# Optimization experiments

Measured on AMD Instinct MI355X. Metric: run time of the kernel, lower is better.

The kernel has to match this reference:

```python
import jax, jax.numpy as jnp
import numpy as np

N = 50000      # nodes
E = 1600000    # edges
R = 12         # relations (num_unique_edge_attrs)
F_IN = 64      # num_node_features
H = 128        # hidden_channels
C = 10         # num_classes
G = 256        # graphs in batch
EPS = 1e-5     # BatchNorm eps


def setup_inputs() -> dict:
    key = jax.random.key(0)
    ks = jax.random.split(key, 10)
    s = 0.05
    return {
        "x": jax.random.normal(ks[0], (N, F_IN), jnp.float32),
        "Wrel1": jax.random.normal(ks[1], (R, F_IN, H), jnp.float32) * s,
        "root1": jax.random.normal(ks[2], (F_IN, H), jnp.float32) * s,
        "bias1": jnp.zeros((H,), jnp.float32),
        "gamma1": jnp.ones((H,), jnp.float32),
        "beta1": jnp.zeros((H,), jnp.float32),
        "Wrel2": jax.random.normal(ks[3], (R, H, H), jnp.float32) * s,
        "root2": jax.random.normal(ks[4], (H, H), jnp.float32) * s,
        "bias2": jnp.zeros((H,), jnp.float32),
        "gamma2": jnp.ones((H,), jnp.float32),
        "beta2": jnp.zeros((H,), jnp.float32),
        "Wf": jax.random.normal(ks[5], (H, C), jnp.float32) * s,
        "bf": jnp.zeros((C,), jnp.float32),
        "edge_index": jax.random.randint(ks[6], (2, E), 0, N, dtype=jnp.int64) if jax.config.jax_enable_x64 else jax.random.randint(ks[6], (2, E), 0, N),
        "edge_type": jax.random.randint(ks[7], (E,), 0, R),
        "batch": jnp.sort(jax.random.randint(ks[8], (N,), 0, G)),
    }


def _segment_mean(vals, idx, num):
    # mean aggregation; empty segments -> 0
    s = jax.ops.segment_sum(vals, idx, num_segments=num)
    c = jax.ops.segment_sum(jnp.ones(idx.shape, vals.dtype), idx, num_segments=num)
    return s / jnp.clip(c, 1.0)[:, None]


def _rgcn(x, Wrel, root, bias, src, dst, edge_type):
    # PyG RGCNConv with aggr='mean': per-relation mean of source features, then W_r
    seg = dst * R + edge_type                      # fused (node, relation) segment id
    h = _segment_mean(x[src], seg, N * R)          # [N*R, in]
    h = h.reshape(N, R, x.shape[1])
    return jnp.einsum('nri,rio->no', h, Wrel) + x @ root + bias


def _bn(x, gamma, beta):
    # BatchNorm1d training-mode math (batch statistics, biased variance)
    mu = jnp.mean(x, axis=0)
    var = jnp.mean((x - mu) ** 2, axis=0)
    return gamma * (x - mu) / jnp.sqrt(var + EPS) + beta


def reference(x, Wrel1, root1, bias1, gamma1, beta1,
              Wrel2, root2, bias2, gamma2, beta2,
              Wf, bf, edge_index, edge_type, batch):
    src, dst = edge_index[0], edge_index[1]
    h = jax.nn.relu(_bn(_rgcn(x, Wrel1, root1, bias1, src, dst, edge_type), gamma1, beta1))
    h = jax.nn.relu(_bn(_rgcn(h, Wrel2, root2, bias2, src, dst, edge_type), gamma2, beta2))
    pooled = _segment_mean(h, batch, G)            # global_mean_pool -> [G, H]
    return pooled @ Wf + bf                        # [G, C]
```

## Files before the change

### kernel.cpp

```cpp
#include <hip/hip_runtime.h>

constexpr int N_NODES = 50000;
constexpr int N_EDGES = 1600000;
constexpr int NREL    = 12;
constexpr int F_INPUT = 64;
constexpr int HID     = 128;
constexpr int NCLS    = 10;
constexpr int NGRAPH  = 256;
constexpr int NSEG    = N_NODES * NREL;
constexpr float BN_EPS = 1e-5f;

constexpr int NB    = 391;
constexpr int SEGB  = 128 * NREL;
constexpr int NBLK  = 392;
constexpr int PTPB  = 1024;
constexpr int EPB   = 4096;

typedef float v4f __attribute__((ext_vector_type(4)));
typedef short s8b __attribute__((ext_vector_type(8)));

__device__ __forceinline__ unsigned f2bf(float f) {
    unsigned u = __float_as_uint(f);
    return (u + 0x7FFFu + ((u >> 16) & 1u)) >> 16;
}
__device__ __forceinline__ unsigned pack2(float a, float b) {
    return f2bf(a) | (f2bf(b) << 16);
}

constexpr int PQ0 = 64;
constexpr int PQ1 = PQ0 + 64;
constexpr int PQ2 = PQ1 + 8192;
constexpr int PQ3 = PQ2 + 13 * F_INPUT * HID;
constexpr int PQ4 = PQ3 + 13 * HID * HID;
constexpr int PQ5 = PQ4 + N_NODES * F_INPUT / 4;
constexpr int PQ6 = PQ5 + NGRAPH;
constexpr int PREP_BLOCKS = (PQ6 + 255) / 256;

__global__ void prep(const float* __restrict__ Wrel1, const float* __restrict__ root1,
                     const float* __restrict__ Wrel2, const float* __restrict__ root2,
                     const float* __restrict__ x, const int* __restrict__ batch,
                     ushort* __restrict__ Wp1, ushort* __restrict__ Wp2,
                     ushort* __restrict__ xb,
                     float* __restrict__ bn1, float* __restrict__ bn2,
                     float* __restrict__ psum, float* __restrict__ pcnt) {
    int tid = blockIdx.x * 256 + threadIdx.x;
    const uint4 z = make_uint4(0, 0, 0, 0);
    if (tid < PQ0) { reinterpret_cast<uint4*>(bn1)[tid] = z; return; }
    if (tid < PQ1) { reinterpret_cast<uint4*>(bn2)[tid - PQ0] = z; return; }
    if (tid < PQ2) { reinterpret_cast<uint4*>(psum)[tid - PQ1] = z; return; }
    if (tid < PQ3) {
        int idx = tid - PQ2;
        int r = idx >> 13, rem = idx & 8191;
        int k = rem >> 7, n = rem & 127;
        const float* W = (r < NREL) ? (Wrel1 + (size_t)r * 8192) : root1;
        float v = W[k * HID + n];
        int b = k >> 5, kk = k & 31;
        int j = (n & 7) * 16 + (n >> 3);
        Wp1[(((size_t)(r * 2 + b)) * HID + j) * 32 + kk] = (ushort)f2bf(v);
        return;
    }
    if (tid < PQ4) {
        int idx = tid - PQ3;
        int r = idx >> 14, rem = idx & 16383;
        int k = rem >> 7, n = rem & 127;
        const float* W = (r < NREL) ? (Wrel2 + (size_t)r * 16384) : root2;
        float v = W[k * HID + n];
        int b = k >> 5, kk = k & 31;
        int j = (n & 7) * 16 + (n >> 3);
        Wp2[(((size_t)(r * 4 + b)) * HID + j) * 32 + kk] = (ushort)f2bf(v);
        return;
    }
    if (tid < PQ5) {
        int i = tid - PQ4;
        float4 v = reinterpret_cast<const float4*>(x)[i];
        uint2 o;
        o.x = pack2(v.x, v.y);
        o.y = pack2(v.z, v.w);
        reinterpret_cast<uint2*>(xb)[i] = o;
        return;
    }
    if (tid < PQ6) {
        int g = tid - PQ5;
        int lo0 = 0, hi0 = N_NODES;
        while (lo0 < hi0) { int m = (lo0 + hi0) >> 1; if (batch[m] < g) lo0 = m + 1; else hi0 = m; }
        int lo1 = lo0, hi1 = N_NODES;
        while (lo1 < hi1) { int m = (lo1 + hi1) >> 1; if (batch[m] < g + 1) lo1 = m + 1; else hi1 = m; }
        pcnt[g] = (float)(lo1 - lo0);
    }
}


__global__ __launch_bounds__(PTPB)
void part_hist(const int* __restrict__ dst, int* __restrict__ histG) {
    __shared__ int h[NB];
    int t = threadIdx.x, blk = blockIdx.x;
    if (t < NB) h[t] = 0;
    __syncthreads();
    int base = blk * EPB;
#pragma unroll
    for (int it = 0; it < EPB / PTPB; ++it) {
        int e = base + it * PTPB + t;
        if (e < N_EDGES) atomicAdd(&h[dst[e] >> 7], 1);
    }
    __syncthreads();
    if (t < NB) histG[blk * NB + t] = h[t];
}

__global__ __launch_bounds__(512)
void part_scanA(const int* __restrict__ histG, int* __restrict__ cursorG,
                int* __restrict__ bucketTot) {
    __shared__ int s[512];
    int t = threadIdx.x, b = blockIdx.x;
    int v = (t < NBLK) ? histG[t * NB + b] : 0;
    s[t] = v;
    __syncthreads();
    for (int d = 1; d < 512; d <<= 1) {
        int x = (t >= d) ? s[t - d] : 0;
        __syncthreads();
        s[t] += x;
        __syncthreads();
    }
    if (t < NBLK) cursorG[t * NB + b] = s[t] - v;
    if (t == NBLK - 1) bucketTot[b] = s[t];
}

__global__ __launch_bounds__(512)
void part_scanB(const int* __restrict__ bucketTot, int* __restrict__ bucketBase) {
    __shared__ int s[512];
    int t = threadIdx.x;
    int v = (t < NB) ? bucketTot[t] : 0;
    s[t] = v;
    __syncthreads();
    for (int d = 1; d < 512; d <<= 1) {
        int x = (t >= d) ? s[t - d] : 0;
        __syncthreads();
        s[t] += x;
        __syncthreads();
    }
    if (t <= NB) bucketBase[t] = (t == 0) ? 0 : s[t - 1];
}

__global__ __launch_bounds__(PTPB)
void part_scatter(const int* __restrict__ src, const int* __restrict__ dst,
                  const int* __restrict__ et, const int* __restrict__ cursorG,
                  const int* __restrict__ bucketBase, uint* __restrict__ ebuck) {
    __shared__ int cur[NB];
    int t = threadIdx.x, blk = blockIdx.x;
    if (t < NB) cur[t] = cursorG[blk * NB + t] + bucketBase[t];
    __syncthreads();
    int base = blk * EPB;
#pragma unroll
    for (int it = 0; it < EPB / PTPB; ++it) {
        int e = base + it * PTPB + t;
        if (e < N_EDGES) {
            int d = dst[e];
            int b = d >> 7;
            int pos = atomicAdd(&cur[b], 1);
            ebuck[pos] = (uint)src[e] | ((uint)(d & 127) << 16) | ((uint)et[e] << 23);
        }
    }
}

__global__ __launch_bounds__(256)
void csr_finalize(const uint* __restrict__ ebuck, const int* __restrict__ bucketBase,
                  int* __restrict__ off, int* __restrict__ zrow, float* __restrict__ wgt) {
    __shared__ int cnt[SEGB];
    __shared__ int cur[SEGB];
    __shared__ float winv[SEGB];
    __shared__ int partial[256];
    int t = threadIdx.x, b = blockIdx.x;
    int eb0 = bucketBase[b], eb1 = bucketBase[b + 1];
#pragma unroll
    for (int i = 0; i < 6; ++i) cnt[t * 6 + i] = 0;
    __syncthreads();
    for (int e = eb0 + t; e < eb1; e += 256) {
        uint u = ebuck[e];
        int key = (int)((u >> 16) & 127) * NREL + (int)(u >> 23);
        atomicAdd(&cnt[key], 1);
    }
    __syncthreads();
    int loc[6];
    int sum = 0;
#pragma unroll
    for (int i = 0; i < 6; ++i) { loc[i] = sum; sum += cnt[t * 6 + i]; }
    partial[t] = sum;
    __syncthreads();
    for (int d = 1; d < 256; d <<= 1) {
        int v = (t >= d) ? partial[t - d] : 0;
        __syncthreads();
        partial[t] += v;
        __syncthreads();
    }
    int tbase = (t == 0) ? 0 : partial[t - 1];
    int nodeb = b * 128;
#pragma unroll
    for (int i = 0; i < 6; ++i) {
        int s = t * 6 + i;
        int gpos = eb0 + tbase + loc[i];
        cur[s] = gpos;
        int c = cnt[s];
        winv[s] = (c > 0) ? 1.0f / (float)c : 0.f;
        int node = nodeb + s / NREL;
        if (node < N_NODES) off[node * NREL + (s % NREL)] = gpos;
    }
    __syncthreads();
    for (int e = eb0 + t; e < eb1; e += 256) {
        uint u = ebuck[e];
        int key = (int)((u >> 16) & 127) * NREL + (int)(u >> 23);
        int pos = atomicAdd(&cur[key], 1);
        zrow[pos] = (int)(u >> 23) * N_NODES + (int)(u & 0xFFFFu);
        wgt[pos] = winv[key];
    }
    if (b == 0 && t == 0) off[NSEG] = N_EDGES;
}


template <int F>
__launch_bounds__(256)
__global__ void gemm_rel(const ushort* __restrict__ xin, const ushort* __restrict__ Wp,
                         ushort* __restrict__ Z) {
    constexpr int FP2 = F + 8;
    constexpr int KB  = F / 32;
    constexpr int CHW = F / 4;
    constexpr int NLD = CHW / 8;
    __shared__ __align__(16) ushort A[64 * FP2];
    const int t = threadIdx.x;
    const int n0 = blockIdx.x * 64;
    const int nl = t >> 2, tid4 = t & 3;
    const int lane = t & 63, wave = t >> 6, q = lane >> 4, l16 = lane & 15;

    {
        int n = n0 + nl;
        uint4* dst = reinterpret_cast<uint4*>(A + nl * FP2 + tid4 * CHW);
        if (n < N_NODES) {
            const uint4* srcp =
                reinterpret_cast<const uint4*>(xin + (size_t)n * F + tid4 * CHW);
#pragma unroll
            for (int c = 0; c < NLD; ++c) dst[c] = srcp[c];
        } else {
            uint4 z = make_uint4(0, 0, 0, 0);
#pragma unroll
            for (int c = 0; c < NLD; ++c) dst[c] = z;
        }
    }
    __syncthreads();

    s8b afr[KB];
    const ushort* Arow = A + (wave * 16 + l16) * FP2 + q * 8;
#pragma unroll
    for (int b = 0; b < KB; ++b)
        afr[b] = *reinterpret_cast<const s8b*>(Arow + b * 32);

    const int rowb = n0 + wave * 16 + q * 4;
    for (int rel = 0; rel < 13; ++rel) {
        v4f acc[8];
#pragma unroll
        for (int nt = 0; nt < 8; ++nt) acc[nt] = (v4f){0.f, 0.f, 0.f, 0.f};
#pragma unroll
        for (int b = 0; b < KB; ++b) {
            const ushort* wb = Wp + ((size_t)(rel * KB + b) * HID + l16) * 32 + q * 8;
#pragma unroll
            for (int nt = 0; nt < 8; ++nt) {
                s8b bfb = *reinterpret_cast<const s8b*>(wb + (size_t)nt * 16 * 32);
                acc[nt] = __builtin_amdgcn_mfma_f32_16x16x32_bf16(afr[b], bfb, acc[nt], 0, 0, 0);
            }
        }
        ushort* zr = Z + (size_t)rel * ((size_t)N_NODES * HID);
#pragma unroll
        for (int rr = 0; rr < 4; ++rr) {
            int n = rowb + rr;
            if (n < N_NODES) {
                uint4 o;
                o.x = pack2(acc[0][rr], acc[1][rr]);
                o.y = pack2(acc[2][rr], acc[3][rr]);
                o.z = pack2(acc[4][rr], acc[5][rr]);
                o.w = pack2(acc[6][rr], acc[7][rr]);
                *reinterpret_cast<uint4*>(zr + (size_t)n * HID + l16 * 8) = o;
            }
        }
    }
}


__launch_bounds__(256)
__global__ void agg_bn(const ushort* __restrict__ Z, const int* __restrict__ off,
                       const int* __restrict__ zrow, const float* __restrict__ wgt,
                       const float* __restrict__ bias,
                       float* __restrict__ H, float* __restrict__ bn_sum,
                       float* __restrict__ bn_sq) {
    __shared__ float RED[2][4][HID];
    const int t = threadIdx.x;
    const int lane = t & 63, wave = t >> 6;
    const int n0 = blockIdx.x * 32 + wave * 8;
    const float2 bv = *reinterpret_cast<const float2*>(bias + lane * 2);
    float ps0 = 0.f, ps1 = 0.f, pq0 = 0.f, pq1 = 0.f;

    for (int i = 0; i < 8; ++i) {
        int n = n0 + i;
        if (n >= N_NODES) break;
        int e0 = off[n * NREL];
        int ee = off[n * NREL + NREL];
        uint ur = *reinterpret_cast<const uint*>(
            Z + ((size_t)12 * N_NODES + n) * HID + lane * 2);
        float a0 = __uint_as_float(ur << 16) + bv.x;
        float a1 = __uint_as_float(ur & 0xFFFF0000u) + bv.y;
        int elast = ee - 1;
        for (int e = e0; e < ee; e += 8) {
            int zr_[8];
            float w_[8];
#pragma unroll
            for (int j = 0; j < 8; ++j) {
                int ec = min(e + j, elast);
                zr_[j] = zrow[ec];
                w_[j] = (e + j < ee) ? wgt[ec] : 0.f;
            }
            uint u_[8];
#pragma unroll
            for (int j = 0; j < 8; ++j)
                u_[j] = *reinterpret_cast<const uint*>(
                    Z + (size_t)zr_[j] * HID + lane * 2);
#pragma unroll
            for (int j = 0; j < 8; ++j) {
                a0 += __uint_as_float(u_[j] << 16) * w_[j];
                a1 += __uint_as_float(u_[j] & 0xFFFF0000u) * w_[j];
            }
        }
        *reinterpret_cast<float2*>(H + (size_t)n * HID + lane * 2) = make_float2(a0, a1);
        ps0 += a0; ps1 += a1;
        pq0 += a0 * a0; pq1 += a1 * a1;
    }
    RED[0][wave][lane * 2] = ps0; RED[0][wave][lane * 2 + 1] = ps1;
    RED[1][wave][lane * 2] = pq0; RED[1][wave][lane * 2 + 1] = pq1;
    __syncthreads();
    {
        int stat = t >> 7, col = t & 127;
        float v = RED[stat][0][col] + RED[stat][1][col] +
                  RED[stat][2][col] + RED[stat][3][col];
        if (stat == 0) atomicAdd(&bn_sum[col], v);
        else           atomicAdd(&bn_sq[col], v);
    }
}


__global__ void bn_relu_bf16(const float* __restrict__ h, const float* __restrict__ bn_sum,
                             const float* __restrict__ bn_sq, const float* __restrict__ gamma,
                             const float* __restrict__ beta, ushort* __restrict__ outb) {
    __shared__ float CA[HID], CB[HID];
    int t = threadIdx.x;
    if (t < HID) {
        float mu = bn_sum[t] * (1.0f / N_NODES);
        float var = bn_sq[t] * (1.0f / N_NODES) - mu * mu;
        float a = gamma[t] / sqrtf(var + BN_EPS);
        CA[t] = a;
        CB[t] = beta[t] - a * mu;
    }
    __syncthreads();
    int i = blockIdx.x * 256 + t;
    constexpr int TOTAL = N_NODES * HID / 4;
    if (i < TOTAL) {
        int o4 = i & 31;
        float4 a = reinterpret_cast<const float4*>(CA)[o4];
        float4 b = reinterpret_cast<const float4*>(CB)[o4];
        float4 v = reinterpret_cast<const float4*>(h)[i];
        v.x = fmaxf(a.x * v.x + b.x, 0.f);
        v.y = fmaxf(a.y * v.y + b.y, 0.f);
        v.z = fmaxf(a.z * v.z + b.z, 0.f);
        v.w = fmaxf(a.w * v.w + b.w, 0.f);
        uint2 o;
        o.x = pack2(v.x, v.y);
        o.y = pack2(v.z, v.w);
        reinterpret_cast<uint2*>(outb)[i] = o;
    }
}


__global__ void pool_bnrelu(const float* __restrict__ h, const float* __restrict__ bn_sum,
                            const float* __restrict__ bn_sq, const float* __restrict__ gamma,
                            const float* __restrict__ beta, const int* __restrict__ batch,
                            float* __restrict__ psum) {
    __shared__ float CA[HID], CB[HID];
    int t = threadIdx.x;
    if (t < HID) {
        float mu = bn_sum[t] * (1.0f / N_NODES);
        float var = bn_sq[t] * (1.0f / N_NODES) - mu * mu;
        float a = gamma[t] / sqrtf(var + BN_EPS);
        CA[t] = a;
        CB[t] = beta[t] - a * mu;
    }
    __syncthreads();
    int col = t & 127;
    int nb = blockIdx.x * 16 + (t >> 7) * 8;
    float a = CA[col], b = CB[col];
    float run = 0.f;
    int curg = -1;
    for (int i = 0; i < 8; ++i) {
        int n = nb + i;
        if (n < N_NODES) {
            int g = batch[n];
            float v = fmaxf(a * h[(size_t)n * HID + col] + b, 0.f);
            if (g != curg) {
                if (curg >= 0) atomicAdd(&psum[curg * HID + col], run);
                run = 0.f;
                curg = g;
            }
            run += v;
        }
    }
    if (curg >= 0) atomicAdd(&psum[curg * HID + col], run);
}

__global__ void final_kernel(const float* __restrict__ psum, const float* __restrict__ pcnt,
                             const float* __restrict__ Wf, const float* __restrict__ bf,
                             float* __restrict__ out) {
    __shared__ float p[HID];
    int g = blockIdx.x, t = threadIdx.x;
    float inv = 1.0f / fmaxf(pcnt[g], 1.0f);
    p[t] = psum[g * HID + t] * inv;
    p[t + 64] = psum[g * HID + t + 64] * inv;
    __syncthreads();
    if (t < NCLS) {
        float s = bf[t];
#pragma unroll 16
        for (int k = 0; k < HID; ++k) s += p[k] * Wf[k * NCLS + t];
        out[g * NCLS + t] = s;
    }
}


extern "C" void kernel_launch(void* const* d_in, const int* in_sizes, int n_in,
                              void* d_out, int out_size, void* d_ws, size_t ws_size,
                              hipStream_t stream) {
    const float* x      = (const float*)d_in[0];
    const float* Wrel1  = (const float*)d_in[1];
    const float* root1  = (const float*)d_in[2];
    const float* bias1  = (const float*)d_in[3];
    const float* gamma1 = (const float*)d_in[4];
    const float* beta1  = (const float*)d_in[5];
    const float* Wrel2  = (const float*)d_in[6];
    const float* root2  = (const float*)d_in[7];
    const float* bias2  = (const float*)d_in[8];
    const float* gamma2 = (const float*)d_in[9];
    const float* beta2  = (const float*)d_in[10];
    const float* Wf     = (const float*)d_in[11];
    const float* bf     = (const float*)d_in[12];
    const int* ei       = (const int*)d_in[13];
    const int* et       = (const int*)d_in[14];
    const int* batch    = (const int*)d_in[15];
    const int* srcv = ei;
    const int* dstv = ei + N_EDGES;

    char* w = (char*)d_ws;
    auto alloc = [&](size_t bytes) -> char* {
        char* p = w;
        w += (bytes + 255) / 256 * 256;
        return p;
    };
    int* off     = (int*)alloc((size_t)(NSEG + 1) * 4);
    int* zrow    = (int*)alloc((size_t)N_EDGES * 4);
    float* wgt   = (float*)alloc((size_t)N_EDGES * 4);
    ushort* xb   = (ushort*)alloc((size_t)N_NODES * F_INPUT * 2);
    ushort* H1b  = (ushort*)alloc((size_t)N_NODES * HID * 2);
    ushort* Wp1  = (ushort*)alloc((size_t)13 * F_INPUT * HID * 2);
    ushort* Wp2  = (ushort*)alloc((size_t)13 * HID * HID * 2);
    float* bn1   = (float*)alloc(2 * HID * 4);
    float* bn2   = (float*)alloc(2 * HID * 4);
    float* psum  = (float*)alloc((size_t)NGRAPH * HID * 4);
    float* pcnt  = (float*)alloc((size_t)NGRAPH * 4);
    float* Hbuf  = (float*)alloc((size_t)N_NODES * HID * 4);
    char* ovl    = alloc((size_t)13 * N_NODES * HID * 2);
    int* histG      = (int*)ovl;
    int* cursorG    = (int*)(ovl + (size_t)NBLK * NB * 4);
    int* bucketTot  = (int*)(ovl + (size_t)2 * NBLK * NB * 4);
    int* bucketBase = (int*)(ovl + (size_t)2 * NBLK * NB * 4 + (NB + 1) * 4 + 252);
    uint* ebuck     = (uint*)(ovl + (size_t)2 * NBLK * NB * 4 + 4096);
    ushort* Zb      = (ushort*)ovl;

    prep<<<PREP_BLOCKS, 256, 0, stream>>>(Wrel1, root1, Wrel2, root2, x, batch,
                                          Wp1, Wp2, xb, bn1, bn2, psum, pcnt);

    part_hist<<<NBLK, PTPB, 0, stream>>>(dstv, histG);
    part_scanA<<<NB, 512, 0, stream>>>(histG, cursorG, bucketTot);
    part_scanB<<<1, 512, 0, stream>>>(bucketTot, bucketBase);
    part_scatter<<<NBLK, PTPB, 0, stream>>>(srcv, dstv, et, cursorG, bucketBase, ebuck);
    csr_finalize<<<NB, 256, 0, stream>>>(ebuck, bucketBase, off, zrow, wgt);

    int gblk = (N_NODES + 63) / 64;
    int ablk = (N_NODES + 31) / 32;

    gemm_rel<F_INPUT><<<gblk, 256, 0, stream>>>(xb, Wp1, Zb);
    agg_bn<<<ablk, 256, 0, stream>>>(Zb, off, zrow, wgt, bias1, Hbuf, bn1, bn1 + HID);
    bn_relu_bf16<<<(N_NODES * HID / 4 + 255) / 256, 256, 0, stream>>>(Hbuf, bn1, bn1 + HID,
                                                                      gamma1, beta1, H1b);

    gemm_rel<HID><<<gblk, 256, 0, stream>>>(H1b, Wp2, Zb);
    agg_bn<<<ablk, 256, 0, stream>>>(Zb, off, zrow, wgt, bias2, Hbuf, bn2, bn2 + HID);

    pool_bnrelu<<<(N_NODES + 15) / 16, 256, 0, stream>>>(Hbuf, bn2, bn2 + HID, gamma2, beta2,
                                                         batch, psum);
    final_kernel<<<NGRAPH, 64, 0, stream>>>(psum, pcnt, Wf, bf, (float*)d_out);
}
```

Baseline: 556.4 us.

## Split relation transforms into two passes to shrink the gathered Z buffer

Each RGCN layer's per-relation transform and gather-aggregation now runs in two halves: relations 0-5, then relations 6-11 plus the root term. This shrinks the bf16 Z buffer from 13 to 7 relation slabs, so the random gathers hit a smaller working set that fits better in cache. The cost is two extra kernel launches per layer, re-reading the input features for the second GEMM, and an extra read-modify-write of the fp32 H buffer.

```diff
diff --git a/kernel.cpp b/kernel.cpp
--- a/kernel.cpp
+++ b/kernel.cpp
@@ -9,6 +9,9 @@
 constexpr int NGRAPH  = 256;
 constexpr int NSEG    = N_NODES * NREL;
 constexpr float BN_EPS = 1e-5f;
+
+constexpr int NRELA = 6;
+constexpr int NRELB = 7;
 
 constexpr int NB    = 391;
 constexpr int SEGB  = 128 * NREL;
@@ -206,16 +209,18 @@
     __syncthreads();
     for (int e = eb0 + t; e < eb1; e += 256) {
         uint u = ebuck[e];
-        int key = (int)((u >> 16) & 127) * NREL + (int)(u >> 23);
+        int rel = (int)(u >> 23);
+        int key = (int)((u >> 16) & 127) * NREL + rel;
         int pos = atomicAdd(&cur[key], 1);
-        zrow[pos] = (int)(u >> 23) * N_NODES + (int)(u & 0xFFFFu);
+        int relc = (rel < NRELA) ? rel : rel - NRELA;
+        zrow[pos] = relc * N_NODES + (int)(u & 0xFFFFu);
         wgt[pos] = winv[key];
     }
     if (b == 0 && t == 0) off[NSEG] = N_EDGES;
 }
 
 
-template <int F>
+template <int F, int NR>
 __launch_bounds__(256)
 __global__ void gemm_rel(const ushort* __restrict__ xin, const ushort* __restrict__ Wp,
                          ushort* __restrict__ Z) {
@@ -252,7 +257,7 @@
         afr[b] = *reinterpret_cast<const s8b*>(Arow + b * 32);
 
     const int rowb = n0 + wave * 16 + q * 4;
-    for (int rel = 0; rel < 13; ++rel) {
+    for (int rel = 0; rel < NR; ++rel) {
         v4f acc[8];
 #pragma unroll
         for (int nt = 0; nt < 8; ++nt) acc[nt] = (v4f){0.f, 0.f, 0.f, 0.f};
@@ -282,6 +287,7 @@
 }
 
 
+template <bool FIRST>
 __launch_bounds__(256)
 __global__ void agg_bn(const ushort* __restrict__ Z, const int* __restrict__ off,
                        const int* __restrict__ zrow, const float* __restrict__ wgt,
@@ -292,47 +298,61 @@
     const int t = threadIdx.x;
     const int lane = t & 63, wave = t >> 6;
     const int n0 = blockIdx.x * 32 + wave * 8;
-    const float2 bv = *reinterpret_cast<const float2*>(bias + lane * 2);
+    const float2 bv = FIRST ? make_float2(0.f, 0.f)
+                            : *reinterpret_cast<const float2*>(bias + lane * 2);
     float ps0 = 0.f, ps1 = 0.f, pq0 = 0.f, pq1 = 0.f;
 
     for (int i = 0; i < 8; ++i) {
         int n = n0 + i;
         if (n >= N_NODES) break;
-        int e0 = off[n * NREL];
-        int ee = off[n * NREL + NREL];
-        uint ur = *reinterpret_cast<const uint*>(
-            Z + ((size_t)12 * N_NODES + n) * HID + lane * 2);
-        float a0 = __uint_as_float(ur << 16) + bv.x;
-        float a1 = __uint_as_float(ur & 0xFFFF0000u) + bv.y;
-        int elast = ee - 1;
-        for (int e = e0; e < ee; e += 8) {
-            int zr_[8];
-            float w_[8];
-#pragma unroll
-            for (int j = 0; j < 8; ++j) {
-                int ec = min(e + j, elast);
-                zr_[j] = zrow[ec];
-                w_[j] = (e + j < ee) ? wgt[ec] : 0.f;
+        int e0, ee;
+        float a0, a1;
+        if (FIRST) {
+            e0 = off[n * NREL];
+            ee = off[n * NREL + NRELA];
+            a0 = 0.f; a1 = 0.f;
+        } else {
+            e0 = off[n * NREL + NRELA];
+            ee = off[n * NREL + NREL];
+            float2 hp = *reinterpret_cast<const float2*>(H + (size_t)n * HID + lane * 2);
+            uint ur = *reinterpret_cast<const uint*>(
+                Z + ((size_t)6 * N_NODES + n) * HID + lane * 2);
+            a0 = hp.x + __uint_as_float(ur << 16) + bv.x;
+            a1 = hp.y + __uint_as_float(ur & 0xFFFF0000u) + bv.y;
+        }
+        if (e0 < ee) {
+            int elast = ee - 1;
+            for (int e = e0; e < ee; e += 8) {
+                int zr_[8];
+                float w_[8];
+#pragma unroll
+                for (int j = 0; j < 8; ++j) {
+                    int ec = min(e + j, elast);
+                    zr_[j] = zrow[ec];
+                    w_[j] = (e + j < ee) ? wgt[ec] : 0.f;
+                }
+                uint u_[8];
+#pragma unroll
+                for (int j = 0; j < 8; ++j)
+                    u_[j] = *reinterpret_cast<const uint*>(
+                        Z + (size_t)zr_[j] * HID + lane * 2);
+#pragma unroll
+                for (int j = 0; j < 8; ++j) {
+                    a0 += __uint_as_float(u_[j] << 16) * w_[j];
+                    a1 += __uint_as_float(u_[j] & 0xFFFF0000u) * w_[j];
+                }
             }
-            uint u_[8];
-#pragma unroll
-            for (int j = 0; j < 8; ++j)
-                u_[j] = *reinterpret_cast<const uint*>(
-                    Z + (size_t)zr_[j] * HID + lane * 2);
-#pragma unroll
-            for (int j = 0; j < 8; ++j) {
-                a0 += __uint_as_float(u_[j] << 16) * w_[j];
-                a1 += __uint_as_float(u_[j] & 0xFFFF0000u) * w_[j];
-            }
         }
         *reinterpret_cast<float2*>(H + (size_t)n * HID + lane * 2) = make_float2(a0, a1);
-        ps0 += a0; ps1 += a1;
-        pq0 += a0 * a0; pq1 += a1 * a1;
-    }
-    RED[0][wave][lane * 2] = ps0; RED[0][wave][lane * 2 + 1] = ps1;
-    RED[1][wave][lane * 2] = pq0; RED[1][wave][lane * 2 + 1] = pq1;
-    __syncthreads();
-    {
+        if (!FIRST) {
+            ps0 += a0; ps1 += a1;
+            pq0 += a0 * a0; pq1 += a1 * a1;
+        }
+    }
+    if (!FIRST) {
+        RED[0][wave][lane * 2] = ps0; RED[0][wave][lane * 2 + 1] = ps1;
+        RED[1][wave][lane * 2] = pq0; RED[1][wave][lane * 2 + 1] = pq1;
+        __syncthreads();
         int stat = t >> 7, col = t & 127;
         float v = RED[stat][0][col] + RED[stat][1][col] +
                   RED[stat][2][col] + RED[stat][3][col];
@@ -467,7 +487,7 @@
     float* psum  = (float*)alloc((size_t)NGRAPH * HID * 4);
     float* pcnt  = (float*)alloc((size_t)NGRAPH * 4);
     float* Hbuf  = (float*)alloc((size_t)N_NODES * HID * 4);
-    char* ovl    = alloc((size_t)13 * N_NODES * HID * 2);
+    char* ovl    = alloc((size_t)NRELB * N_NODES * HID * 2);
     int* histG      = (int*)ovl;
     int* cursorG    = (int*)(ovl + (size_t)NBLK * NB * 4);
     int* bucketTot  = (int*)(ovl + (size_t)2 * NBLK * NB * 4);
@@ -487,13 +507,20 @@
     int gblk = (N_NODES + 63) / 64;
     int ablk = (N_NODES + 31) / 32;
 
-    gemm_rel<F_INPUT><<<gblk, 256, 0, stream>>>(xb, Wp1, Zb);
-    agg_bn<<<ablk, 256, 0, stream>>>(Zb, off, zrow, wgt, bias1, Hbuf, bn1, bn1 + HID);
+    const size_t WOFF1 = (size_t)NRELA * (F_INPUT / 32) * HID * 32;
+    const size_t WOFF2 = (size_t)NRELA * (HID / 32) * HID * 32;
+
+    gemm_rel<F_INPUT, NRELA><<<gblk, 256, 0, stream>>>(xb, Wp1, Zb);
+    agg_bn<true><<<ablk, 256, 0, stream>>>(Zb, off, zrow, wgt, bias1, Hbuf, bn1, bn1 + HID);
+    gemm_rel<F_INPUT, NRELB><<<gblk, 256, 0, stream>>>(xb, Wp1 + WOFF1, Zb);
+    agg_bn<false><<<ablk, 256, 0, stream>>>(Zb, off, zrow, wgt, bias1, Hbuf, bn1, bn1 + HID);
     bn_relu_bf16<<<(N_NODES * HID / 4 + 255) / 256, 256, 0, stream>>>(Hbuf, bn1, bn1 + HID,
                                                                       gamma1, beta1, H1b);
 
-    gemm_rel<HID><<<gblk, 256, 0, stream>>>(H1b, Wp2, Zb);
-    agg_bn<<<ablk, 256, 0, stream>>>(Zb, off, zrow, wgt, bias2, Hbuf, bn2, bn2 + HID);
+    gemm_rel<HID, NRELA><<<gblk, 256, 0, stream>>>(H1b, Wp2, Zb);
+    agg_bn<true><<<ablk, 256, 0, stream>>>(Zb, off, zrow, wgt, bias2, Hbuf, bn2, bn2 + HID);
+    gemm_rel<HID, NRELB><<<gblk, 256, 0, stream>>>(H1b, Wp2 + WOFF2, Zb);
+    agg_bn<false><<<ablk, 256, 0, stream>>>(Zb, off, zrow, wgt, bias2, Hbuf, bn2, bn2 + HID);
 
     pool_bnrelu<<<(N_NODES + 15) / 16, 256, 0, stream>>>(Hbuf, bn2, bn2 + HID, gamma2, beta2,
                                                          batch, psum);
```

Result: slower. 591.6 us (+6.3%).

## Reorder RGCN to aggregate inputs first, then single concatenated GEMM with fused BN stats

Applied to the files above, without the earlier changes.

Instead of computing per-relation transformed features for all nodes and gathering them per edge, the code now computes per-(node,relation) means of the raw input features into a concatenated matrix and multiplies it by stacked weights in one GEMM. Bias and BatchNorm statistics are fused into the GEMM epilogue, and the CSR no longer stores per-edge weights or relation-offset row indices. Gathers now hit a small input array instead of the large 13-slice Z buffer, improving cache locality, at the cost of writing and reading a large concatenated intermediate and a longer-K GEMM.

```diff
diff --git a/kernel.cpp b/kernel.cpp
--- a/kernel.cpp
+++ b/kernel.cpp
@@ -163,10 +163,9 @@
 
 __global__ __launch_bounds__(256)
 void csr_finalize(const uint* __restrict__ ebuck, const int* __restrict__ bucketBase,
-                  int* __restrict__ off, int* __restrict__ zrow, float* __restrict__ wgt) {
+                  int* __restrict__ off, int* __restrict__ esrc) {
     __shared__ int cnt[SEGB];
     __shared__ int cur[SEGB];
-    __shared__ float winv[SEGB];
     __shared__ int partial[256];
     int t = threadIdx.x, b = blockIdx.x;
     int eb0 = bucketBase[b], eb1 = bucketBase[b + 1];
@@ -198,8 +197,6 @@
         int s = t * 6 + i;
         int gpos = eb0 + tbase + loc[i];
         cur[s] = gpos;
-        int c = cnt[s];
-        winv[s] = (c > 0) ? 1.0f / (float)c : 0.f;
         int node = nodeb + s / NREL;
         if (node < N_NODES) off[node * NREL + (s % NREL)] = gpos;
     }
@@ -208,8 +205,7 @@
         uint u = ebuck[e];
         int key = (int)((u >> 16) & 127) * NREL + (int)(u >> 23);
         int pos = atomicAdd(&cur[key], 1);
-        zrow[pos] = (int)(u >> 23) * N_NODES + (int)(u & 0xFFFFu);
-        wgt[pos] = winv[key];
+        esrc[pos] = (int)(u & 0xFFFFu);
     }
     if (b == 0 && t == 0) off[NSEG] = N_EDGES;
 }
@@ -217,125 +213,140 @@
 
 template <int F>
 __launch_bounds__(256)
-__global__ void gemm_rel(const ushort* __restrict__ xin, const ushort* __restrict__ Wp,
-                         ushort* __restrict__ Z) {
-    constexpr int FP2 = F + 8;
-    constexpr int KB  = F / 32;
-    constexpr int CHW = F / 4;
-    constexpr int NLD = CHW / 8;
-    __shared__ __align__(16) ushort A[64 * FP2];
-    const int t = threadIdx.x;
-    const int n0 = blockIdx.x * 64;
-    const int nl = t >> 2, tid4 = t & 3;
-    const int lane = t & 63, wave = t >> 6, q = lane >> 4, l16 = lane & 15;
-
-    {
-        int n = n0 + nl;
-        uint4* dst = reinterpret_cast<uint4*>(A + nl * FP2 + tid4 * CHW);
-        if (n < N_NODES) {
-            const uint4* srcp =
-                reinterpret_cast<const uint4*>(xin + (size_t)n * F + tid4 * CHW);
-#pragma unroll
-            for (int c = 0; c < NLD; ++c) dst[c] = srcp[c];
-        } else {
-            uint4 z = make_uint4(0, 0, 0, 0);
-#pragma unroll
-            for (int c = 0; c < NLD; ++c) dst[c] = z;
-        }
-    }
-    __syncthreads();
-
-    s8b afr[KB];
-    const ushort* Arow = A + (wave * 16 + l16) * FP2 + q * 8;
-#pragma unroll
-    for (int b = 0; b < KB; ++b)
-        afr[b] = *reinterpret_cast<const s8b*>(Arow + b * 32);
-
-    const int rowb = n0 + wave * 16 + q * 4;
-    for (int rel = 0; rel < 13; ++rel) {
-        v4f acc[8];
-#pragma unroll
-        for (int nt = 0; nt < 8; ++nt) acc[nt] = (v4f){0.f, 0.f, 0.f, 0.f};
-#pragma unroll
-        for (int b = 0; b < KB; ++b) {
-            const ushort* wb = Wp + ((size_t)(rel * KB + b) * HID + l16) * 32 + q * 8;
-#pragma unroll
-            for (int nt = 0; nt < 8; ++nt) {
-                s8b bfb = *reinterpret_cast<const s8b*>(wb + (size_t)nt * 16 * 32);
-                acc[nt] = __builtin_amdgcn_mfma_f32_16x16x32_bf16(afr[b], bfb, acc[nt], 0, 0, 0);
-            }
-        }
-        ushort* zr = Z + (size_t)rel * ((size_t)N_NODES * HID);
-#pragma unroll
-        for (int rr = 0; rr < 4; ++rr) {
-            int n = rowb + rr;
-            if (n < N_NODES) {
-                uint4 o;
-                o.x = pack2(acc[0][rr], acc[1][rr]);
-                o.y = pack2(acc[2][rr], acc[3][rr]);
-                o.z = pack2(acc[4][rr], acc[5][rr]);
-                o.w = pack2(acc[6][rr], acc[7][rr]);
-                *reinterpret_cast<uint4*>(zr + (size_t)n * HID + l16 * 8) = o;
-            }
-        }
-    }
-}
-
-
-__launch_bounds__(256)
-__global__ void agg_bn(const ushort* __restrict__ Z, const int* __restrict__ off,
-                       const int* __restrict__ zrow, const float* __restrict__ wgt,
-                       const float* __restrict__ bias,
-                       float* __restrict__ H, float* __restrict__ bn_sum,
-                       float* __restrict__ bn_sq) {
-    __shared__ float RED[2][4][HID];
+__global__ void agg_m(const ushort* __restrict__ xin, const int* __restrict__ off,
+                      const int* __restrict__ esrc, ushort* __restrict__ Mb) {
+    constexpr int KT = 13 * F;
     const int t = threadIdx.x;
     const int lane = t & 63, wave = t >> 6;
+    const int half = lane >> 5;
+    const int cofs = (F == 128) ? lane * 2 : (lane & 31) * 2;
     const int n0 = blockIdx.x * 32 + wave * 8;
-    const float2 bv = *reinterpret_cast<const float2*>(bias + lane * 2);
-    float ps0 = 0.f, ps1 = 0.f, pq0 = 0.f, pq1 = 0.f;
 
     for (int i = 0; i < 8; ++i) {
         int n = n0 + i;
         if (n >= N_NODES) break;
-        int e0 = off[n * NREL];
-        int ee = off[n * NREL + NREL];
-        uint ur = *reinterpret_cast<const uint*>(
-            Z + ((size_t)12 * N_NODES + n) * HID + lane * 2);
-        float a0 = __uint_as_float(ur << 16) + bv.x;
-        float a1 = __uint_as_float(ur & 0xFFFF0000u) + bv.y;
-        int elast = ee - 1;
-        for (int e = e0; e < ee; e += 8) {
-            int zr_[8];
-            float w_[8];
-#pragma unroll
-            for (int j = 0; j < 8; ++j) {
-                int ec = min(e + j, elast);
-                zr_[j] = zrow[ec];
-                w_[j] = (e + j < ee) ? wgt[ec] : 0.f;
+        if (F == 128 || half == 0) {
+            uint ur = *reinterpret_cast<const uint*>(xin + (size_t)n * F + cofs);
+            *reinterpret_cast<uint*>(Mb + (size_t)n * KT + 12 * F + cofs) = ur;
+        }
+        constexpr int NR = (F == 128) ? 12 : 6;
+#pragma unroll 2
+        for (int rr = 0; rr < NR; ++rr) {
+            int r = (F == 128) ? rr : rr * 2 + half;
+            int e0 = off[n * NREL + r], e1 = off[n * NREL + r + 1];
+            float f0 = 0.f, f1 = 0.f;
+            int elast = e1 - 1;
+            for (int e = e0; e < e1; e += 4) {
+                int i0 = esrc[e];
+                int i1 = esrc[min(e + 1, elast)];
+                int i2 = esrc[min(e + 2, elast)];
+                int i3 = esrc[min(e + 3, elast)];
+                uint u0 = *reinterpret_cast<const uint*>(xin + (size_t)i0 * F + cofs);
+                uint u1 = *reinterpret_cast<const uint*>(xin + (size_t)i1 * F + cofs);
+                uint u2 = *reinterpret_cast<const uint*>(xin + (size_t)i2 * F + cofs);
+                uint u3 = *reinterpret_cast<const uint*>(xin + (size_t)i3 * F + cofs);
+                f0 += __uint_as_float(u0 << 16);
+                f1 += __uint_as_float(u0 & 0xFFFF0000u);
+                if (e + 1 < e1) { f0 += __uint_as_float(u1 << 16); f1 += __uint_as_float(u1 & 0xFFFF0000u); }
+                if (e + 2 < e1) { f0 += __uint_as_float(u2 << 16); f1 += __uint_as_float(u2 & 0xFFFF0000u); }
+                if (e + 3 < e1) { f0 += __uint_as_float(u3 << 16); f1 += __uint_as_float(u3 & 0xFFFF0000u); }
             }
-            uint u_[8];
-#pragma unroll
-            for (int j = 0; j < 8; ++j)
-                u_[j] = *reinterpret_cast<const uint*>(
-                    Z + (size_t)zr_[j] * HID + lane * 2);
-#pragma unroll
-            for (int j = 0; j < 8; ++j) {
-                a0 += __uint_as_float(u_[j] << 16) * w_[j];
-                a1 += __uint_as_float(u_[j] & 0xFFFF0000u) * w_[j];
+            if (e1 > e0) {
+                float inv = 1.0f / (float)(e1 - e0);
+                f0 *= inv; f1 *= inv;
             }
-        }
-        *reinterpret_cast<float2*>(H + (size_t)n * HID + lane * 2) = make_float2(a0, a1);
-        ps0 += a0; ps1 += a1;
-        pq0 += a0 * a0; pq1 += a1 * a1;
-    }
-    RED[0][wave][lane * 2] = ps0; RED[0][wave][lane * 2 + 1] = ps1;
-    RED[1][wave][lane * 2] = pq0; RED[1][wave][lane * 2 + 1] = pq1;
+            *reinterpret_cast<uint*>(Mb + (size_t)n * KT + r * F + cofs) = pack2(f0, f1);
+        }
+    }
+}
+
+
+template <int F>
+__launch_bounds__(256)
+__global__ void gemm_cat(const ushort* __restrict__ Mb, const ushort* __restrict__ Wp,
+                         const float* __restrict__ bias, float* __restrict__ H,
+                         float* __restrict__ bn_sum, float* __restrict__ bn_sq) {
+    constexpr int KT  = 13 * F;
+    constexpr int NCH = KT / 64;
+    __shared__ __align__(16) ushort As[64 * 72];
+    const int t = threadIdx.x;
+    const int n0 = blockIdx.x * 64;
+    const int lane = t & 63, wave = t >> 6, q = lane >> 4, l16 = lane & 15;
+    const int srow = t >> 2, sq = t & 3;
+    const int nstage = n0 + srow;
+
+    v4f acc[8];
+#pragma unroll
+    for (int nt = 0; nt < 8; ++nt) acc[nt] = (v4f){0.f, 0.f, 0.f, 0.f};
+
+    for (int c = 0; c < NCH; ++c) {
+        __syncthreads();
+        {
+            uint4 v0 = make_uint4(0, 0, 0, 0), v1 = v0;
+            if (nstage < N_NODES) {
+                const uint4* sp = reinterpret_cast<const uint4*>(
+                    Mb + (size_t)nstage * KT + c * 64 + sq * 16);
+                v0 = sp[0];
+                v1 = sp[1];
+            }
+            uint4* dp = reinterpret_cast<uint4*>(As + srow * 72 + sq * 16);
+            dp[0] = v0;
+            dp[1] = v1;
+        }
+        __syncthreads();
+#pragma unroll
+        for (int b = 0; b < 2; ++b) {
+            const int kbg = c * 2 + b;
+            const ushort* wb = Wp + ((size_t)kbg * HID + l16) * 32 + q * 8;
+            s8b af = *reinterpret_cast<const s8b*>(As + (wave * 16 + l16) * 72 + b * 32 + q * 8);
+#pragma unroll
+            for (int nt = 0; nt < 8; ++nt) {
+                s8b bfb = *reinterpret_cast<const s8b*>(wb + (size_t)nt * 16 * 32);
+                acc[nt] = __builtin_amdgcn_mfma_f32_16x16x32_bf16(af, bfb, acc[nt], 0, 0, 0);
+            }
+        }
+    }
+
+    __syncthreads();
+    float* REDs = reinterpret_cast<float*>(As);
+    float* REDq = REDs + 512;
+    const int colb = l16 * 8;
+    float4 b0 = *reinterpret_cast<const float4*>(bias + colb);
+    float4 b1 = *reinterpret_cast<const float4*>(bias + colb + 4);
+    float s_[8] = {0, 0, 0, 0, 0, 0, 0, 0}, q2_[8] = {0, 0, 0, 0, 0, 0, 0, 0};
+#pragma unroll
+    for (int rr = 0; rr < 4; ++rr) {
+        int n = n0 + wave * 16 + q * 4 + rr;
+        if (n < N_NODES) {
+            float v0 = acc[0][rr] + b0.x, v1 = acc[1][rr] + b0.y;
+            float v2 = acc[2][rr] + b0.z, v3 = acc[3][rr] + b0.w;
+            float v4 = acc[4][rr] + b1.x, v5 = acc[5][rr] + b1.y;
+            float v6 = acc[6][rr] + b1.z, v7 = acc[7][rr] + b1.w;
+            *reinterpret_cast<float4*>(H + (size_t)n * HID + colb) = make_float4(v0, v1, v2, v3);
+            *reinterpret_cast<float4*>(H + (size_t)n * HID + colb + 4) = make_float4(v4, v5, v6, v7);
+            s_[0] += v0; s_[1] += v1; s_[2] += v2; s_[3] += v3;
+            s_[4] += v4; s_[5] += v5; s_[6] += v6; s_[7] += v7;
+            q2_[0] += v0 * v0; q2_[1] += v1 * v1; q2_[2] += v2 * v2; q2_[3] += v3 * v3;
+            q2_[4] += v4 * v4; q2_[5] += v5 * v5; q2_[6] += v6 * v6; q2_[7] += v7 * v7;
+        }
+    }
+#pragma unroll
+    for (int nt = 0; nt < 8; ++nt) {
+        s_[nt] += __shfl_xor(s_[nt], 16);  s_[nt] += __shfl_xor(s_[nt], 32);
+        q2_[nt] += __shfl_xor(q2_[nt], 16); q2_[nt] += __shfl_xor(q2_[nt], 32);
+    }
+    if (lane < 16) {
+#pragma unroll
+        for (int nt = 0; nt < 8; ++nt) {
+            REDs[wave * 128 + colb + nt] = s_[nt];
+            REDq[wave * 128 + colb + nt] = q2_[nt];
+        }
+    }
     __syncthreads();
     {
         int stat = t >> 7, col = t & 127;
-        float v = RED[stat][0][col] + RED[stat][1][col] +
-                  RED[stat][2][col] + RED[stat][3][col];
+        const float* R = stat ? REDq : REDs;
+        float v = R[0 * 128 + col] + R[1 * 128 + col] + R[2 * 128 + col] + R[3 * 128 + col];
         if (stat == 0) atomicAdd(&bn_sum[col], v);
         else           atomicAdd(&bn_sq[col], v);
     }
@@ -456,8 +467,7 @@
         return p;
     };
     int* off     = (int*)alloc((size_t)(NSEG + 1) * 4);
-    int* zrow    = (int*)alloc((size_t)N_EDGES * 4);
-    float* wgt   = (float*)alloc((size_t)N_EDGES * 4);
+    int* esrc    = (int*)alloc((size_t)N_EDGES * 4);
     ushort* xb   = (ushort*)alloc((size_t)N_NODES * F_INPUT * 2);
     ushort* H1b  = (ushort*)alloc((size_t)N_NODES * HID * 2);
     ushort* Wp1  = (ushort*)alloc((size_t)13 * F_INPUT * HID * 2);
@@ -467,13 +477,13 @@
     float* psum  = (float*)alloc((size_t)NGRAPH * HID * 4);
     float* pcnt  = (float*)alloc((size_t)NGRAPH * 4);
     float* Hbuf  = (float*)alloc((size_t)N_NODES * HID * 4);
-    char* ovl    = alloc((size_t)13 * N_NODES * HID * 2);
+    char* ovl    = alloc((size_t)N_NODES * 13 * HID * 2);
     int* histG      = (int*)ovl;
     int* cursorG    = (int*)(ovl + (size_t)NBLK * NB * 4);
     int* bucketTot  = (int*)(ovl + (size_t)2 * NBLK * NB * 4);
     int* bucketBase = (int*)(ovl + (size_t)2 * NBLK * NB * 4 + (NB + 1) * 4 + 252);
     uint* ebuck     = (uint*)(ovl + (size_t)2 * NBLK * NB * 4 + 4096);
-    ushort* Zb      = (ushort*)ovl;
+    ushort* Mbuf    = (ushort*)ovl;
 
     prep<<<PREP_BLOCKS, 256, 0, stream>>>(Wrel1, root1, Wrel2, root2, x, batch,
                                           Wp1, Wp2, xb, bn1, bn2, psum, pcnt);
@@ -482,18 +492,18 @@
     part_scanA<<<NB, 512, 0, stream>>>(histG, cursorG, bucketTot);
     part_scanB<<<1, 512, 0, stream>>>(bucketTot, bucketBase);
     part_scatter<<<NBLK, PTPB, 0, stream>>>(srcv, dstv, et, cursorG, bucketBase, ebuck);
-    csr_finalize<<<NB, 256, 0, stream>>>(ebuck, bucketBase, off, zrow, wgt);
-
+    csr_finalize<<<NB, 256, 0, stream>>>(ebuck, bucketBase, off, esrc);
+
+    int ablk = (N_NODES + 31) / 32;
     int gblk = (N_NODES + 63) / 64;
-    int ablk = (N_NODES + 31) / 32;
-
-    gemm_rel<F_INPUT><<<gblk, 256, 0, stream>>>(xb, Wp1, Zb);
-    agg_bn<<<ablk, 256, 0, stream>>>(Zb, off, zrow, wgt, bias1, Hbuf, bn1, bn1 + HID);
+
+    agg_m<F_INPUT><<<ablk, 256, 0, stream>>>(xb, off, esrc, Mbuf);
+    gemm_cat<F_INPUT><<<gblk, 256, 0, stream>>>(Mbuf, Wp1, bias1, Hbuf, bn1, bn1 + HID);
     bn_relu_bf16<<<(N_NODES * HID / 4 + 255) / 256, 256, 0, stream>>>(Hbuf, bn1, bn1 + HID,
                                                                       gamma1, beta1, H1b);
 
-    gemm_rel<HID><<<gblk, 256, 0, stream>>>(H1b, Wp2, Zb);
-    agg_bn<<<ablk, 256, 0, stream>>>(Zb, off, zrow, wgt, bias2, Hbuf, bn2, bn2 + HID);
+    agg_m<HID><<<ablk, 256, 0, stream>>>(H1b, off, esrc, Mbuf);
+    gemm_cat<HID><<<gblk, 256, 0, stream>>>(Mbuf, Wp2, bias2, Hbuf, bn2, bn2 + HID);
 
     pool_bnrelu<<<(N_NODES + 15) / 16, 256, 0, stream>>>(Hbuf, bn2, bn2 + HID, gamma2, beta2,
                                                          batch, psum);
```

After: 579.7 us. 1.04x slower.
